# Kernel optimization log

Hardware: AMD Instinct MI355X
Metric: run time of the kernel (lower is better)

Reference implementation:

```python
import jax, jax.numpy as jnp
import numpy as np

BN_EPS = 1e-5


def _posit_intervals():
    # Replicates conditions_l1 / conditions_g1 interval tables (128 steps each).
    l1, g1 = [], []
    for e in range(16):
        for j in range(8):
            if j == 0:
                l1.append((0.0, 1.0625 / 2**16, 1.0 / 2**16))
            else:
                lo = (1.0625 + 0.125 * (j - 1)) / 2 ** (16 - e)
                hi = (1.0625 + 0.125 * j) / 2 ** (16 - e)
                l1.append((lo, hi, 0.5 * (lo + hi)))
            lo = (1.0625 + 0.125 * (j - 1)) * 2 ** e
            hi = (1.0625 + 0.125 * j) * 2 ** e
            g1.append((lo, hi, 0.5 * (lo + hi)))  # note: j==8 branch in torch code is dead
    return l1, g1

_L1, _G1 = _posit_intervals()


def posit_quantize(x):
    # Faithful emulation of the 128 sequential torch.where passes.
    ax = jnp.abs(x)          # conditions are fixed from the ORIGINAL tensor
    neg = x < 0
    y = x
    for (lo1, hi1, m1), (log_, hig, mg) in zip(_L1, _G1):
        c1 = jnp.logical_and(ax > lo1, ax < hi1)
        cg = jnp.logical_and(ax > log_, ax < hig)
        v1 = jnp.where(neg, -m1, m1).astype(x.dtype)
        vg = jnp.where(neg, -mg, mg).astype(x.dtype)
        # |y| < 1 gate uses the CURRENT tensor, as in the torch loop
        y = jnp.where(jnp.abs(y) < 1, jnp.where(c1, v1, y), jnp.where(cg, vg, y))
    return y


def conv1x1(x, w, b):
    # x: [N,C,D,H,W], w: [O,C] (kernel_size=1), b: [O]
    return jnp.einsum('ncdhw,oc->nodhw', x, w) + b[None, :, None, None, None]


def batchnorm(x, gamma, beta, mean, var):
    inv = gamma / jnp.sqrt(var + BN_EPS)
    return x * inv[None, :, None, None, None] + (beta - mean * inv)[None, :, None, None, None]


def setup_inputs() -> dict:
    key = jax.random.key(0)
    ks = jax.random.split(key, 12)
    C = 256
    x = jax.random.normal(ks[0], (8, C, 16, 32, 32), dtype=jnp.float32)
    w1 = jax.random.normal(ks[1], (C, C), dtype=jnp.float32) * 0.05
    b1 = jax.random.normal(ks[2], (C,), dtype=jnp.float32) * 0.05
    w2 = jax.random.normal(ks[3], (C, C), dtype=jnp.float32) * 0.05
    b2 = jax.random.normal(ks[4], (C,), dtype=jnp.float32) * 0.05
    g1 = jax.random.uniform(ks[5], (C,)) + 0.5
    be1 = jax.random.normal(ks[6], (C,)) * 0.1
    m1 = jax.random.normal(ks[7], (C,)) * 0.1
    v1 = jax.random.uniform(ks[8], (C,)) + 0.5
    g2 = jax.random.uniform(ks[9], (C,)) + 0.5
    be2 = jax.random.normal(ks[10], (C,)) * 0.1
    m2 = jax.random.normal(ks[11], (C,)) * 0.1
    v2 = jax.random.uniform(jax.random.fold_in(key, 99), (C,)) + 0.5
    return {"x": x, "w1": w1, "b1": b1, "g1": g1, "be1": be1, "m1": m1, "v1": v1,
            "w2": w2, "b2": b2, "g2": g2, "be2": be2, "m2": m2, "v2": v2}


def reference(x, w1, b1, g1, be1, m1, v1, w2, b2, g2, be2, m2, v2):
    residual = x
    out = conv1x1(posit_quantize(x), posit_quantize(w1), b1)
    out = jax.nn.relu(batchnorm(out, g1, be1, m1, v1))
    out = conv1x1(posit_quantize(out), posit_quantize(w2), b2)
    out = batchnorm(out, g2, be2, m2, v2)
    return jax.nn.relu(out + residual)
```

## Files before the change

kernel.cpp:

```cpp
#include <hip/hip_runtime.h>

typedef __attribute__((ext_vector_type(8))) short short8;
typedef __attribute__((ext_vector_type(4))) short s4v;
typedef __attribute__((ext_vector_type(4))) float floatx4;

#define SPOS 16384

__device__ __forceinline__ unsigned short f2bf(float f) {
    unsigned u = __float_as_uint(f);
    u += 0x7fffu + ((u >> 16) & 1u);
    return (unsigned short)(u >> 16);
}

__device__ __forceinline__ float posit_q(float x) {
    unsigned xu  = __float_as_uint(x);
    unsigned sgn = xu & 0x80000000u;
    unsigned au  = xu & 0x7fffffffu;
    unsigned m   = au & 0x007fffffu;
    unsigned r   = (au + 0x00080000u) & 0xfff00000u;
    bool bdry = (m & 0x000fffffu) == 0x00080000u;
    unsigned res;
    if (au >= 0x3f800000u) {
        res = r;
        if (m > 0x00700000u && m < 0x00780000u && au < 0x47700000u)
            res = (au & 0xff800000u) + 0x00800000u;
        if ((bdry && m != 0x00780000u) || au >= 0x47780000u)
            res = au;
    } else {
        res = (m <= 0x00080000u || m >= 0x00780000u || bdry) ? au : r;
        if (au < 0x37880000u) res = au ? 0x37800000u : 0u;
    }
    return __uint_as_float(sgn | res);
}

__device__ __forceinline__ float posit_q_pos(float z) {
    unsigned au  = __float_as_uint(z);
    unsigned m   = au & 0x007fffffu;
    unsigned r   = (au + 0x00080000u) & 0xfff00000u;
    bool bdry = (m & 0x000fffffu) == 0x00080000u;
    unsigned res;
    if (au >= 0x3f800000u) {
        res = r;
        if (m > 0x00700000u && m < 0x00780000u && au < 0x47700000u)
            res = (au & 0xff800000u) + 0x00800000u;
        if ((bdry && m != 0x00780000u) || au >= 0x47780000u)
            res = au;
    } else {
        res = (m <= 0x00080000u || m >= 0x00780000u || bdry) ? au : r;
        if (au < 0x37880000u) res = au ? 0x37800000u : 0u;
    }
    return __uint_as_float(res);
}

__global__ __launch_bounds__(256) void prep_kernel(
    const float* __restrict__ w1, const float* __restrict__ w2,
    const float* __restrict__ b1, const float* __restrict__ g1,
    const float* __restrict__ be1, const float* __restrict__ m1,
    const float* __restrict__ v1,
    const float* __restrict__ b2, const float* __restrict__ g2,
    const float* __restrict__ be2, const float* __restrict__ m2,
    const float* __restrict__ v2,
    unsigned short* __restrict__ w1p, unsigned short* __restrict__ w2p,
    float* __restrict__ cst)
{
    int i = blockIdx.x * 256 + threadIdx.x;
    if (i < 65536) {
        const int j    = i & 7;
        const int lane = (i >> 3) & 63;
        const int kb   = (i >> 9) & 7;
        const int G    = i >> 12;
        const int row  = 16 * G + (lane & 15);
        const int k    = 32 * kb + 8 * (lane >> 4) + j;
        w1p[i] = f2bf(posit_q(w1[row * 256 + k]));
        w2p[i] = f2bf(posit_q(w2[row * 256 + k]));
        if (i < 256) {
            float inv1 = g1[i] / sqrtf(v1[i] + 1e-5f);
            cst[i]       = inv1;
            cst[256 + i] = fmaf(b1[i], inv1, be1[i] - m1[i] * inv1);
            float inv2 = g2[i] / sqrtf(v2[i] + 1e-5f);
            cst[512 + i] = inv2;
            cst[768 + i] = fmaf(b2[i], inv2, be2[i] - m2[i] * inv2);
        }
    }
}

__device__ __forceinline__ int qidx(int p, int cb) {
    return p * 256 + ((cb ^ (p & 31)) << 3);
}

__global__ __launch_bounds__(256, 3) void fused_kernel(
    const float* __restrict__ x,
    const unsigned short* __restrict__ w1p,
    const unsigned short* __restrict__ w2p,
    const float* __restrict__ cst,
    float* __restrict__ out)
{
    __shared__ alignas(16) unsigned short q[64 * 256];
    __shared__ alignas(16) float xs[4 * 1024];

    const int b  = blockIdx.x;
    const int n  = b >> 8;
    const int s0 = (b & 255) << 6;
    const float* xb = x   + (size_t)n * (256 * SPOS) + s0;
    float*       ob = out + (size_t)n * (256 * SPOS) + s0;

    const int t    = threadIdx.x;
    const int lane = t & 63;
    const int w    = t >> 6;
    const int quad = lane >> 4;
    const int l15  = lane & 15;

    {
        const int g  = lane & 15;
        const int co = lane >> 4;
        float* xsw = xs + w * 1024;
        const float* src0 = xb + (size_t)(64 * w + co) * SPOS + 4 * g;
        float4 v[16];
        #pragma unroll
        for (int r = 0; r < 8; ++r) {
            v[2 * r]     = *(const float4*)(src0 + (size_t)(8 * r) * SPOS);
            v[2 * r + 1] = *(const float4*)(src0 + (size_t)(8 * r + 4) * SPOS);
        }
        #pragma unroll
        for (int r = 0; r < 8; ++r) {
            float* xr = xsw + (r & 1) * 512;
            *(float4*)&xr[co * 64 + ((4 * g) ^ (4 * co))]             = v[2 * r];
            *(float4*)&xr[(co + 4) * 64 + ((4 * g) ^ (4 * (co + 4)))] = v[2 * r + 1];
            short8 pk;
            #pragma unroll
            for (int c8 = 0; c8 < 8; ++c8)
                pk[c8] = (short)f2bf(posit_q(xr[c8 * 64 + (lane ^ (4 * c8))]));
            *(short8*)&q[qidx(lane, 8 * w + r)] = pk;
        }
    }
    __syncthreads();

    floatx4 acc[4][4];
    #pragma unroll
    for (int i = 0; i < 4; ++i)
        #pragma unroll
        for (int jj = 0; jj < 4; ++jj)
            acc[i][jj] = (floatx4)0.0f;

    #pragma unroll
    for (int kk = 0; kk < 256; kk += 32) {
        short8 af[4], bf[4];
        #pragma unroll
        for (int i = 0; i < 4; ++i)
            af[i] = *(const short8*)&w1p[(((w * 4 + i) * 8 + (kk >> 5)) * 64 + lane) * 8];
        #pragma unroll
        for (int jj = 0; jj < 4; ++jj)
            bf[jj] = *(const short8*)&q[qidx(16 * jj + l15, (kk >> 3) + quad)];
        #pragma unroll
        for (int i = 0; i < 4; ++i)
            #pragma unroll
            for (int jj = 0; jj < 4; ++jj)
                acc[i][jj] = __builtin_amdgcn_mfma_f32_16x16x32_bf16(af[i], bf[jj], acc[i][jj], 0, 0, 0);
    }

    short8 af20[4];
    #pragma unroll
    for (int i = 0; i < 4; ++i)
        af20[i] = *(const short8*)&w2p[(((w * 4 + i) * 8 + 0) * 64 + lane) * 8];

    __syncthreads();

    const int mbase = w * 64;

    {
        const float* sc1 = cst;
        const float* bi1 = cst + 256;
        #pragma unroll
        for (int i = 0; i < 4; ++i) {
            const int m0 = mbase + 16 * i + quad * 4;
            float sc[4], bi[4];
            #pragma unroll
            for (int r = 0; r < 4; ++r) { sc[r] = sc1[m0 + r]; bi[r] = bi1[m0 + r]; }
            #pragma unroll
            for (int jj = 0; jj < 4; ++jj) {
                const int p = 16 * jj + l15;
                s4v h;
                #pragma unroll
                for (int r = 0; r < 4; ++r) {
                    float z = fmaf(acc[i][jj][r], sc[r], bi[r]);
                    z = fmaxf(z, 0.0f);
                    h[r] = (short)f2bf(posit_q_pos(z));
                }
                *(s4v*)&q[qidx(p, m0 >> 3) + (m0 & 7)] = h;
            }
        }
    }
    __syncthreads();

    #pragma unroll
    for (int i = 0; i < 4; ++i)
        #pragma unroll
        for (int jj = 0; jj < 4; ++jj)
            acc[i][jj] = (floatx4)0.0f;

    #pragma unroll
    for (int kk = 0; kk < 256; kk += 32) {
        short8 af[4], bf[4];
        #pragma unroll
        for (int i = 0; i < 4; ++i)
            af[i] = (kk == 0) ? af20[i]
                  : *(const short8*)&w2p[(((w * 4 + i) * 8 + (kk >> 5)) * 64 + lane) * 8];
        #pragma unroll
        for (int jj = 0; jj < 4; ++jj)
            bf[jj] = *(const short8*)&q[qidx(16 * jj + l15, (kk >> 3) + quad)];
        #pragma unroll
        for (int i = 0; i < 4; ++i)
            #pragma unroll
            for (int jj = 0; jj < 4; ++jj)
                acc[i][jj] = __builtin_amdgcn_mfma_f32_16x16x32_bf16(af[i], bf[jj], acc[i][jj], 0, 0, 0);
    }

    {
        const float* sc2 = cst + 512;
        const float* bi2 = cst + 768;
        #pragma unroll
        for (int i = 0; i < 4; ++i) {
            const int m0 = mbase + 16 * i + quad * 4;
            float sc[4], bi[4];
            #pragma unroll
            for (int r = 0; r < 4; ++r) { sc[r] = sc2[m0 + r]; bi[r] = bi2[m0 + r]; }
            #pragma unroll
            for (int jj = 0; jj < 4; ++jj) {
                const int p = 16 * jj + l15;
                #pragma unroll
                for (int r = 0; r < 4; ++r) {
                    const size_t off = (size_t)(m0 + r) * SPOS + p;
                    float v = fmaf(acc[i][jj][r], sc[r], bi[r]);
                    v += xb[off];
                    ob[off] = fmaxf(v, 0.0f);
                }
            }
        }
    }
}

extern "C" void kernel_launch(void* const* d_in, const int* in_sizes, int n_in,
                              void* d_out, int out_size, void* d_ws, size_t ws_size,
                              hipStream_t stream) {
    const float* x   = (const float*)d_in[0];
    const float* w1  = (const float*)d_in[1];
    const float* b1  = (const float*)d_in[2];
    const float* g1  = (const float*)d_in[3];
    const float* be1 = (const float*)d_in[4];
    const float* m1  = (const float*)d_in[5];
    const float* v1  = (const float*)d_in[6];
    const float* w2  = (const float*)d_in[7];
    const float* b2  = (const float*)d_in[8];
    const float* g2  = (const float*)d_in[9];
    const float* be2 = (const float*)d_in[10];
    const float* m2  = (const float*)d_in[11];
    const float* v2  = (const float*)d_in[12];

    unsigned short* w1p = (unsigned short*)d_ws;
    unsigned short* w2p = w1p + 65536;
    float* cst = (float*)(w2p + 65536);

    prep_kernel<<<256, 256, 0, stream>>>(w1, w2, b1, g1, be1, m1, v1,
                                         b2, g2, be2, m2, v2, w1p, w2p, cst);
    fused_kernel<<<2048, 256, 0, stream>>>(x, w1p, w2p, cst, (float*)d_out);
}
```

Baseline: 348.4 us.

## Vectorize epilogue via swapped MFMA operands, shrink staging LDS, raise occupancy

The second GEMM's MFMA operands are swapped so each lane holds four consecutive spatial positions for one channel. This lets the epilogue load the residual and store the output as float4 instead of scalar strided accesses. The x staging buffer is halved by reusing one 512-float slot per wave, with loads for rows r+4 issued while earlier rows are processed. Launch bounds rise to 4 blocks per SM to allow more occupancy, which risks register pressure and spills.

```diff
diff --git a/kernel.cpp b/kernel.cpp
--- a/kernel.cpp
+++ b/kernel.cpp
@@ -88,7 +88,7 @@
     return p * 256 + ((cb ^ (p & 31)) << 3);
 }
 
-__global__ __launch_bounds__(256, 3) void fused_kernel(
+__global__ __launch_bounds__(256, 4) void fused_kernel(
     const float* __restrict__ x,
     const unsigned short* __restrict__ w1p,
     const unsigned short* __restrict__ w2p,
@@ -96,7 +96,7 @@
     float* __restrict__ out)
 {
     __shared__ alignas(16) unsigned short q[64 * 256];
-    __shared__ alignas(16) float xs[4 * 1024];
+    __shared__ alignas(16) float xs[4 * 512];
 
     const int b  = blockIdx.x;
     const int n  = b >> 8;
@@ -113,23 +113,28 @@
     {
         const int g  = lane & 15;
         const int co = lane >> 4;
-        float* xsw = xs + w * 1024;
+        float* xsw = xs + w * 512;
         const float* src0 = xb + (size_t)(64 * w + co) * SPOS + 4 * g;
-        float4 v[16];
-        #pragma unroll
-        for (int r = 0; r < 8; ++r) {
+        float4 v[8];
+        #pragma unroll
+        for (int r = 0; r < 4; ++r) {
             v[2 * r]     = *(const float4*)(src0 + (size_t)(8 * r) * SPOS);
             v[2 * r + 1] = *(const float4*)(src0 + (size_t)(8 * r + 4) * SPOS);
         }
         #pragma unroll
         for (int r = 0; r < 8; ++r) {
-            float* xr = xsw + (r & 1) * 512;
-            *(float4*)&xr[co * 64 + ((4 * g) ^ (4 * co))]             = v[2 * r];
-            *(float4*)&xr[(co + 4) * 64 + ((4 * g) ^ (4 * (co + 4)))] = v[2 * r + 1];
+            float4 a0 = v[2 * (r & 3)];
+            float4 a1 = v[2 * (r & 3) + 1];
+            if (r < 4) {
+                v[2 * (r & 3)]     = *(const float4*)(src0 + (size_t)(8 * (r + 4)) * SPOS);
+                v[2 * (r & 3) + 1] = *(const float4*)(src0 + (size_t)(8 * (r + 4) + 4) * SPOS);
+            }
+            *(float4*)&xsw[co * 64 + ((4 * g) ^ (4 * co))]             = a0;
+            *(float4*)&xsw[(co + 4) * 64 + ((4 * g) ^ (4 * (co + 4)))] = a1;
             short8 pk;
             #pragma unroll
             for (int c8 = 0; c8 < 8; ++c8)
-                pk[c8] = (short)f2bf(posit_q(xr[c8 * 64 + (lane ^ (4 * c8))]));
+                pk[c8] = (short)f2bf(posit_q(xsw[c8 * 64 + (lane ^ (4 * c8))]));
             *(short8*)&q[qidx(lane, 8 * w + r)] = pk;
         }
     }
@@ -212,7 +217,7 @@
         for (int i = 0; i < 4; ++i)
             #pragma unroll
             for (int jj = 0; jj < 4; ++jj)
-                acc[i][jj] = __builtin_amdgcn_mfma_f32_16x16x32_bf16(af[i], bf[jj], acc[i][jj], 0, 0, 0);
+                acc[i][jj] = __builtin_amdgcn_mfma_f32_16x16x32_bf16(bf[jj], af[i], acc[i][jj], 0, 0, 0);
     }
 
     {
@@ -220,20 +225,21 @@
         const float* bi2 = cst + 768;
         #pragma unroll
         for (int i = 0; i < 4; ++i) {
-            const int m0 = mbase + 16 * i + quad * 4;
-            float sc[4], bi[4];
-            #pragma unroll
-            for (int r = 0; r < 4; ++r) { sc[r] = sc2[m0 + r]; bi[r] = bi2[m0 + r]; }
+            const int ch = mbase + 16 * i + l15;
+            const float sc = sc2[ch];
+            const float bi = bi2[ch];
+            const float* xr = xb + (size_t)ch * SPOS + 4 * quad;
+            float*       orow = ob + (size_t)ch * SPOS + 4 * quad;
             #pragma unroll
             for (int jj = 0; jj < 4; ++jj) {
-                const int p = 16 * jj + l15;
+                float4 res = *(const float4*)(xr + 16 * jj);
+                float4 o;
                 #pragma unroll
                 for (int r = 0; r < 4; ++r) {
-                    const size_t off = (size_t)(m0 + r) * SPOS + p;
-                    float v = fmaf(acc[i][jj][r], sc[r], bi[r]);
-                    v += xb[off];
-                    ob[off] = fmaxf(v, 0.0f);
+                    float v2 = fmaf(acc[i][jj][r], sc, bi) + ((const float*)&res)[r];
+                    ((float*)&o)[r] = fmaxf(v2, 0.0f);
                 }
+                *(float4*)(orow + 16 * jj) = o;
             }
         }
     }
```

Measured after the change: 350.1 us. Within noise of the previous version (+0.5%).

## Transpose second GEMM operands for vectorized epilogue, double-buffer weight fragment loads

Applied to the files above, without the earlier changes.

The second MFMA swaps its A and B operands, so each lane holds four consecutive spatial positions of a single channel. This lets the epilogue load the residual and write the output as 16-byte vectors, using nontemporal stores instead of scattered scalar accesses. Both GEMM loops now double-buffer the weight fragments, loading the next k-step while the current MFMAs run, and the residual loads are hoisted ahead of the arithmetic. In exchange the kernel holds more registers for the prefetch buffers and the residual tile, which may lower occupancy.

```diff
diff --git a/kernel.cpp b/kernel.cpp
--- a/kernel.cpp
+++ b/kernel.cpp
@@ -115,17 +115,17 @@
         const int co = lane >> 4;
         float* xsw = xs + w * 1024;
         const float* src0 = xb + (size_t)(64 * w + co) * SPOS + 4 * g;
-        float4 v[16];
+        floatx4 v[16];
         #pragma unroll
         for (int r = 0; r < 8; ++r) {
-            v[2 * r]     = *(const float4*)(src0 + (size_t)(8 * r) * SPOS);
-            v[2 * r + 1] = *(const float4*)(src0 + (size_t)(8 * r + 4) * SPOS);
+            v[2 * r]     = *(const floatx4*)(src0 + (size_t)(8 * r) * SPOS);
+            v[2 * r + 1] = *(const floatx4*)(src0 + (size_t)(8 * r + 4) * SPOS);
         }
         #pragma unroll
         for (int r = 0; r < 8; ++r) {
             float* xr = xsw + (r & 1) * 512;
-            *(float4*)&xr[co * 64 + ((4 * g) ^ (4 * co))]             = v[2 * r];
-            *(float4*)&xr[(co + 4) * 64 + ((4 * g) ^ (4 * (co + 4)))] = v[2 * r + 1];
+            *(floatx4*)&xr[co * 64 + ((4 * g) ^ (4 * co))]             = v[2 * r];
+            *(floatx4*)&xr[(co + 4) * 64 + ((4 * g) ^ (4 * (co + 4)))] = v[2 * r + 1];
             short8 pk;
             #pragma unroll
             for (int c8 = 0; c8 < 8; ++c8)
@@ -142,20 +142,28 @@
         for (int jj = 0; jj < 4; ++jj)
             acc[i][jj] = (floatx4)0.0f;
 
-    #pragma unroll
-    for (int kk = 0; kk < 256; kk += 32) {
-        short8 af[4], bf[4];
+    {
+        short8 af[2][4], bf[4];
         #pragma unroll
         for (int i = 0; i < 4; ++i)
-            af[i] = *(const short8*)&w1p[(((w * 4 + i) * 8 + (kk >> 5)) * 64 + lane) * 8];
-        #pragma unroll
-        for (int jj = 0; jj < 4; ++jj)
-            bf[jj] = *(const short8*)&q[qidx(16 * jj + l15, (kk >> 3) + quad)];
-        #pragma unroll
-        for (int i = 0; i < 4; ++i)
+            af[0][i] = *(const short8*)&w1p[(((w * 4 + i) * 8 + 0) * 64 + lane) * 8];
+        #pragma unroll
+        for (int kk = 0; kk < 8; ++kk) {
+            const int cur = kk & 1, nxt = cur ^ 1;
+            if (kk < 7) {
+                #pragma unroll
+                for (int i = 0; i < 4; ++i)
+                    af[nxt][i] = *(const short8*)&w1p[(((w * 4 + i) * 8 + (kk + 1)) * 64 + lane) * 8];
+            }
             #pragma unroll
             for (int jj = 0; jj < 4; ++jj)
-                acc[i][jj] = __builtin_amdgcn_mfma_f32_16x16x32_bf16(af[i], bf[jj], acc[i][jj], 0, 0, 0);
+                bf[jj] = *(const short8*)&q[qidx(16 * jj + l15, 4 * kk + quad)];
+            #pragma unroll
+            for (int i = 0; i < 4; ++i)
+                #pragma unroll
+                for (int jj = 0; jj < 4; ++jj)
+                    acc[i][jj] = __builtin_amdgcn_mfma_f32_16x16x32_bf16(af[cur][i], bf[jj], acc[i][jj], 0, 0, 0);
+        }
     }
 
     short8 af20[4];
@@ -198,42 +206,57 @@
         for (int jj = 0; jj < 4; ++jj)
             acc[i][jj] = (floatx4)0.0f;
 
-    #pragma unroll
-    for (int kk = 0; kk < 256; kk += 32) {
-        short8 af[4], bf[4];
+    {
+        short8 af[2][4], bf[4];
         #pragma unroll
         for (int i = 0; i < 4; ++i)
-            af[i] = (kk == 0) ? af20[i]
-                  : *(const short8*)&w2p[(((w * 4 + i) * 8 + (kk >> 5)) * 64 + lane) * 8];
-        #pragma unroll
-        for (int jj = 0; jj < 4; ++jj)
-            bf[jj] = *(const short8*)&q[qidx(16 * jj + l15, (kk >> 3) + quad)];
-        #pragma unroll
-        for (int i = 0; i < 4; ++i)
+            af[0][i] = af20[i];
+        #pragma unroll
+        for (int kk = 0; kk < 8; ++kk) {
+            const int cur = kk & 1, nxt = cur ^ 1;
+            if (kk < 7) {
+                #pragma unroll
+                for (int i = 0; i < 4; ++i)
+                    af[nxt][i] = *(const short8*)&w2p[(((w * 4 + i) * 8 + (kk + 1)) * 64 + lane) * 8];
+            }
             #pragma unroll
             for (int jj = 0; jj < 4; ++jj)
-                acc[i][jj] = __builtin_amdgcn_mfma_f32_16x16x32_bf16(af[i], bf[jj], acc[i][jj], 0, 0, 0);
+                bf[jj] = *(const short8*)&q[qidx(16 * jj + l15, 4 * kk + quad)];
+            #pragma unroll
+            for (int i = 0; i < 4; ++i)
+                #pragma unroll
+                for (int jj = 0; jj < 4; ++jj)
+                    acc[i][jj] = __builtin_amdgcn_mfma_f32_16x16x32_bf16(bf[jj], af[cur][i], acc[i][jj], 0, 0, 0);
+        }
     }
 
     {
         const float* sc2 = cst + 512;
         const float* bi2 = cst + 768;
+        floatx4 res[4][4];
         #pragma unroll
         for (int i = 0; i < 4; ++i) {
-            const int m0 = mbase + 16 * i + quad * 4;
-            float sc[4], bi[4];
-            #pragma unroll
-            for (int r = 0; r < 4; ++r) { sc[r] = sc2[m0 + r]; bi[r] = bi2[m0 + r]; }
+            const int ch = mbase + 16 * i + l15;
+            const float* xr = xb + (size_t)ch * SPOS + 4 * quad;
+            #pragma unroll
+            for (int jj = 0; jj < 4; ++jj)
+                res[i][jj] = *(const floatx4*)(xr + 16 * jj);
+        }
+        #pragma unroll
+        for (int i = 0; i < 4; ++i) {
+            const int ch = mbase + 16 * i + l15;
+            const float sc = sc2[ch];
+            const float bi = bi2[ch];
+            float* orow = ob + (size_t)ch * SPOS + 4 * quad;
             #pragma unroll
             for (int jj = 0; jj < 4; ++jj) {
-                const int p = 16 * jj + l15;
+                floatx4 o;
                 #pragma unroll
                 for (int r = 0; r < 4; ++r) {
-                    const size_t off = (size_t)(m0 + r) * SPOS + p;
-                    float v = fmaf(acc[i][jj][r], sc[r], bi[r]);
-                    v += xb[off];
-                    ob[off] = fmaxf(v, 0.0f);
+                    float vv = fmaf(acc[i][jj][r], sc, bi) + res[i][jj][r];
+                    o[r] = fmaxf(vv, 0.0f);
                 }
+                __builtin_nontemporal_store(o, (floatx4*)(orow + 16 * jj));
             }
         }
     }
```

After: 340.9 us. 2.1% less time.
